# Kernel tuning notes

Measured on AMD Instinct MI355X. Metric: run time of the kernel, lower is better.

## Reference

```python
import jax, jax.numpy as jnp
import numpy as np

N = 20000      # nodes
E = 200000     # edges
IN = 128       # in_feat
OUT = 128      # out_feat
NB = 8         # num_bases
SI = IN // NB  # submat_in = 16
SO = OUT // NB # submat_out = 16
R = 230        # num_rels
T = 365        # total_times


def setup_inputs() -> dict:
    key = jax.random.key(0)
    ks = jax.random.split(key, 11)
    h = jax.random.normal(ks[0], (N, IN), jnp.float32)
    edge_norm = jax.random.uniform(ks[1], (E, 1), jnp.float32)
    node_norm = jax.random.uniform(ks[2], (N, 1), jnp.float32)
    weight = jax.random.normal(ks[3], (R, NB * SI * SO), jnp.float32) * 0.05
    h_bias = jnp.zeros((OUT,), jnp.float32)
    loop_weight = jax.random.normal(ks[4], (IN, OUT), jnp.float32) * 0.05
    time_embed = jax.random.normal(ks[5], (T, IN), jnp.float32) * 0.05
    edge_src = jax.random.randint(ks[6], (E,), 0, N)
    edge_dst = jax.random.randint(ks[7], (E,), 0, N)
    edge_type = jax.random.randint(ks[8], (E,), 0, R)
    time_idx = jax.random.randint(ks[9], (N,), 0, T)
    return dict(h=h, edge_norm=edge_norm, node_norm=node_norm, weight=weight,
                h_bias=h_bias, loop_weight=loop_weight, time_embed=time_embed,
                edge_src=edge_src, edge_dst=edge_dst, edge_type=edge_type,
                time_idx=time_idx)


def reference(h, edge_norm, node_norm, weight, h_bias, loop_weight, time_embed,
              edge_src, edge_dst, edge_type, time_idx):
    # self-loop message
    loop_message = h @ loop_weight                              # [N, OUT]
    # msg_func: per-edge relation weight gather + block-diagonal bmm
    W_e = weight[edge_type].reshape(-1, NB, SI, SO)             # [E, NB, SI, SO]
    src = h[edge_src].reshape(-1, NB, SI)                       # [E, NB, SI]
    msg = jnp.einsum('ebi,ebio->ebo', src, W_e).reshape(-1, OUT)  # [E, OUT]
    msg = msg * edge_norm
    # fn.sum aggregation over destination nodes
    agg = jax.ops.segment_sum(msg, edge_dst, num_segments=N)    # [N, OUT]
    # apply_func: scale by node norm, then bias + self loop + activation
    node_repr = agg * node_norm
    node_repr = node_repr + h_bias + loop_message
    node_repr = jax.nn.relu(node_repr)
    # get_time_embedding: per-node time embedding gather
    time_embedding = time_embed[time_idx]                       # [N, IN]
    return node_repr, time_embedding
```

## Files before the change

### kernel.cpp

```cpp
#include <hip/hip_runtime.h>
#include <hip/hip_bf16.h>

#define N 20000
#define E 200000
#define IN 128
#define OUT 128
#define NB 8
#define SI 16
#define SO 16
#define R 230
#define T 365

__device__ float g_agg[(size_t)N * OUT];
__device__ int   g_deg[N];
__device__ int   g_off[N + 1];
__device__ int   g_cur[N];
__device__ int   g_srt_src[E];
__device__ int   g_srt_typ[E];
__device__ float g_srt_nrm[E];

__global__ void zero_deg_kernel() {
    int i = blockIdx.x * blockDim.x + threadIdx.x;
    if (i < N) g_deg[i] = 0;
}

__global__ void count_kernel(const int* __restrict__ edge_dst) {
    int e = blockIdx.x * blockDim.x + threadIdx.x;
    if (e < E) atomicAdd(&g_deg[edge_dst[e]], 1);
}

__global__ __launch_bounds__(1024) void scan_kernel() {
    __shared__ int part[1024];
    const int t = threadIdx.x;
    const int base = t * 20;
    int csum = 0;
    int d[20];
#pragma unroll
    for (int k = 0; k < 20; ++k) {
        int idx = base + k;
        d[k] = (idx < N) ? g_deg[idx] : 0;
        csum += d[k];
    }
    part[t] = csum;
    __syncthreads();
    for (int off = 1; off < 1024; off <<= 1) {
        int v = (t >= off) ? part[t - off] : 0;
        __syncthreads();
        part[t] += v;
        __syncthreads();
    }
    int run = part[t] - csum;
#pragma unroll
    for (int k = 0; k < 20; ++k) {
        int idx = base + k;
        if (idx < N) {
            g_off[idx] = run;
            g_cur[idx] = run;
            run += d[k];
        }
    }
    if (t == 1023) g_off[N] = part[1023];
}

__global__ void scatter_kernel(const int* __restrict__ edge_src,
                               const int* __restrict__ edge_dst,
                               const int* __restrict__ edge_type,
                               const float* __restrict__ edge_norm) {
    int e = blockIdx.x * blockDim.x + threadIdx.x;
    if (e >= E) return;
    int pos = atomicAdd(&g_cur[edge_dst[e]], 1);
    g_srt_src[pos] = edge_src[e];
    g_srt_typ[pos] = edge_type[e];
    g_srt_nrm[pos] = edge_norm[e];
}

__global__ __launch_bounds__(128) void agg_kernel(const float* __restrict__ h,
                                                  const float* __restrict__ weight) {
    const int n    = blockIdx.x;
    const int tid  = threadIdx.x;
    const int el   = tid >> 5;
    const int slot = tid & 31;
    const int b    = slot >> 2;
    const int ol0  = (slot & 3) << 2;
    const int j0 = g_off[n], j1 = g_off[n + 1];

    float4 acc = make_float4(0.f, 0.f, 0.f, 0.f);
    for (int j = j0 + el; j < j1; j += 4) {
        int   s  = g_srt_src[j];
        int   r  = g_srt_typ[j];
        float nr = g_srt_nrm[j];
        const float4* hp = reinterpret_cast<const float4*>(h + (long)s * IN + b * SI);
        const float4* wp = reinterpret_cast<const float4*>(
            weight + (long)r * (NB * SI * SO) + b * (SI * SO) + ol0);
        float4 d = make_float4(0.f, 0.f, 0.f, 0.f);
#pragma unroll
        for (int q = 0; q < 4; ++q) {
            float4 hq = hp[q];
            float4 w0 = wp[(4 * q + 0) * 4];
            float4 w1 = wp[(4 * q + 1) * 4];
            float4 w2 = wp[(4 * q + 2) * 4];
            float4 w3 = wp[(4 * q + 3) * 4];
            d.x = fmaf(hq.x, w0.x, d.x); d.y = fmaf(hq.x, w0.y, d.y);
            d.z = fmaf(hq.x, w0.z, d.z); d.w = fmaf(hq.x, w0.w, d.w);
            d.x = fmaf(hq.y, w1.x, d.x); d.y = fmaf(hq.y, w1.y, d.y);
            d.z = fmaf(hq.y, w1.z, d.z); d.w = fmaf(hq.y, w1.w, d.w);
            d.x = fmaf(hq.z, w2.x, d.x); d.y = fmaf(hq.z, w2.y, d.y);
            d.z = fmaf(hq.z, w2.z, d.z); d.w = fmaf(hq.z, w2.w, d.w);
            d.x = fmaf(hq.w, w3.x, d.x); d.y = fmaf(hq.w, w3.y, d.y);
            d.z = fmaf(hq.w, w3.z, d.z); d.w = fmaf(hq.w, w3.w, d.w);
        }
        acc.x = fmaf(d.x, nr, acc.x);
        acc.y = fmaf(d.y, nr, acc.y);
        acc.z = fmaf(d.z, nr, acc.z);
        acc.w = fmaf(d.w, nr, acc.w);
    }

    __shared__ float4 red[128];
    red[tid] = acc;
    __syncthreads();
    if (tid < 64) {
        float4 a = red[tid], c = red[tid + 64];
        a.x += c.x; a.y += c.y; a.z += c.z; a.w += c.w;
        red[tid] = a;
    }
    __syncthreads();
    if (tid < 32) {
        float4 a = red[tid], c = red[tid + 32];
        a.x += c.x; a.y += c.y; a.z += c.z; a.w += c.w;
        reinterpret_cast<float4*>(g_agg)[(long)n * 32 + tid] = a;
    }
}

__global__ __launch_bounds__(128) void node_kernel(
        const float* __restrict__ h,
        const float* __restrict__ node_norm,
        const float* __restrict__ h_bias,
        const float* __restrict__ loop_weight,
        const float* __restrict__ time_embed,
        const int* __restrict__ time_idx,
        float* __restrict__ out) {
    __shared__ float hsm[IN * 16];
    const int tid  = threadIdx.x;
    const int base = blockIdx.x * 16;

    for (int k = tid; k < 16 * IN; k += 128) {
        int nl = k >> 7;
        int i  = k & 127;
        hsm[i * 16 + nl] = h[(long)(base + nl) * IN + i];
    }
    __syncthreads();

    float acc[16];
#pragma unroll
    for (int nl = 0; nl < 16; ++nl) acc[nl] = 0.f;

    for (int i = 0; i < IN; ++i) {
        float w = loop_weight[(long)i * OUT + tid];
        const float4* hp = reinterpret_cast<const float4*>(&hsm[i * 16]);
#pragma unroll
        for (int q = 0; q < 4; ++q) {
            float4 hv = hp[q];
            acc[q * 4 + 0] = fmaf(hv.x, w, acc[q * 4 + 0]);
            acc[q * 4 + 1] = fmaf(hv.y, w, acc[q * 4 + 1]);
            acc[q * 4 + 2] = fmaf(hv.z, w, acc[q * 4 + 2]);
            acc[q * 4 + 3] = fmaf(hv.w, w, acc[q * 4 + 3]);
        }
    }

    float bias = h_bias[tid];
#pragma unroll
    for (int nl = 0; nl < 16; ++nl) {
        int n = base + nl;
        float v = g_agg[(long)n * OUT + tid] * node_norm[n] + bias + acc[nl];
        out[(long)n * OUT + tid] = fmaxf(v, 0.f);
        out[(long)N * OUT + (long)n * IN + tid] =
            time_embed[(long)time_idx[n] * IN + tid];
    }
}

extern "C" void kernel_launch(void* const* d_in, const int* in_sizes, int n_in,
                              void* d_out, int out_size, void* d_ws, size_t ws_size,
                              hipStream_t stream) {
    const float* h           = (const float*)d_in[0];
    const float* edge_norm   = (const float*)d_in[1];
    const float* node_norm   = (const float*)d_in[2];
    const float* weight      = (const float*)d_in[3];
    const float* h_bias      = (const float*)d_in[4];
    const float* loop_weight = (const float*)d_in[5];
    const float* time_embed  = (const float*)d_in[6];
    const int*   edge_src    = (const int*)d_in[7];
    const int*   edge_dst    = (const int*)d_in[8];
    const int*   edge_type   = (const int*)d_in[9];
    const int*   time_idx    = (const int*)d_in[10];
    float* out = (float*)d_out;

    zero_deg_kernel<<<(N + 255) / 256, 256, 0, stream>>>();
    count_kernel<<<(E + 255) / 256, 256, 0, stream>>>(edge_dst);
    scan_kernel<<<1, 1024, 0, stream>>>();
    scatter_kernel<<<(E + 255) / 256, 256, 0, stream>>>(
        edge_src, edge_dst, edge_type, edge_norm);

    agg_kernel<<<N, 128, 0, stream>>>(h, weight);

    node_kernel<<<N / 16, 128, 0, stream>>>(
        h, node_norm, h_bias, loop_weight, time_embed, time_idx, out);
}
```

Baseline: 242.1 us.

## Group edges by relation to reuse weights, materialize messages, then aggregate

Adds a second counting sort of edges by relation type. A new message kernel keeps each relation's weight slice in registers and computes per-edge messages into a global E x OUT buffer at the destination-sorted position. The aggregation kernel then only sums precomputed messages. This removes the repeated per-edge weight gathers, but adds a 100MB message buffer write and read, extra atomics, and a serial per-relation scan.

```diff
diff --git a/kernel.cpp b/kernel.cpp
--- a/kernel.cpp
+++ b/kernel.cpp
@@ -10,23 +10,32 @@
 #define SO 16
 #define R 230
 #define T 365
-
+#define MSG_CHUNKS 8
+
+__device__ float g_msg[(size_t)E * OUT];
 __device__ float g_agg[(size_t)N * OUT];
 __device__ int   g_deg[N];
 __device__ int   g_off[N + 1];
 __device__ int   g_cur[N];
-__device__ int   g_srt_src[E];
-__device__ int   g_srt_typ[E];
-__device__ float g_srt_nrm[E];
-
-__global__ void zero_deg_kernel() {
+__device__ int   g_rdeg[R];
+__device__ int   g_roff[R + 1];
+__device__ int   g_rcur[R];
+__device__ int   g_rsrc[E];
+__device__ int   g_rpos[E];
+__device__ float g_rnrm[E];
+
+__global__ void zero_kernel() {
     int i = blockIdx.x * blockDim.x + threadIdx.x;
     if (i < N) g_deg[i] = 0;
-}
-
-__global__ void count_kernel(const int* __restrict__ edge_dst) {
+    if (i < R) g_rdeg[i] = 0;
+}
+
+__global__ void count_kernel(const int* __restrict__ edge_dst,
+                             const int* __restrict__ edge_type) {
     int e = blockIdx.x * blockDim.x + threadIdx.x;
-    if (e < E) atomicAdd(&g_deg[edge_dst[e]], 1);
+    if (e >= E) return;
+    atomicAdd(&g_deg[edge_dst[e]], 1);
+    atomicAdd(&g_rdeg[edge_type[e]], 1);
 }
 
 __global__ __launch_bounds__(1024) void scan_kernel() {
@@ -60,6 +69,15 @@
         }
     }
     if (t == 1023) g_off[N] = part[1023];
+    if (t == 0) {
+        int acc = 0;
+        for (int r = 0; r < R; ++r) {
+            g_roff[r] = acc;
+            g_rcur[r] = acc;
+            acc += g_rdeg[r];
+        }
+        g_roff[R] = acc;
+    }
 }
 
 __global__ void scatter_kernel(const int* __restrict__ edge_src,
@@ -68,53 +86,73 @@
                                const float* __restrict__ edge_norm) {
     int e = blockIdx.x * blockDim.x + threadIdx.x;
     if (e >= E) return;
-    int pos = atomicAdd(&g_cur[edge_dst[e]], 1);
-    g_srt_src[pos] = edge_src[e];
-    g_srt_typ[pos] = edge_type[e];
-    g_srt_nrm[pos] = edge_norm[e];
-}
-
-__global__ __launch_bounds__(128) void agg_kernel(const float* __restrict__ h,
+    int pd = atomicAdd(&g_cur[edge_dst[e]], 1);
+    int pr = atomicAdd(&g_rcur[edge_type[e]], 1);
+    g_rsrc[pr] = edge_src[e];
+    g_rpos[pr] = pd;
+    g_rnrm[pr] = edge_norm[e];
+}
+
+__global__ __launch_bounds__(256) void msg_kernel(const float* __restrict__ h,
                                                   const float* __restrict__ weight) {
-    const int n    = blockIdx.x;
-    const int tid  = threadIdx.x;
-    const int el   = tid >> 5;
-    const int slot = tid & 31;
-    const int b    = slot >> 2;
-    const int ol0  = (slot & 3) << 2;
+    const int r = blockIdx.x / MSG_CHUNKS;
+    const int c = blockIdx.x % MSG_CHUNKS;
+    const int t = threadIdx.x;
+    const int g = t >> 7;
+    const int o = t & 127;
+    const int b = o >> 4, ol = o & 15;
+
+    const int j0 = g_roff[r], j1 = g_roff[r + 1];
+    const int len = j1 - j0;
+    const int s0 = j0 + (int)(((long)len * c) / MSG_CHUNKS);
+    const int s1 = j0 + (int)(((long)len * (c + 1)) / MSG_CHUNKS);
+
+    float w[SI];
+#pragma unroll
+    for (int i = 0; i < SI; ++i)
+        w[i] = weight[(long)r * (NB * SI * SO) + b * (SI * SO) + i * SO + ol];
+
+    __shared__ float hs[2][IN];
+    for (int base = s0; base < s1; base += 2) {
+        int j = base + g;
+        bool valid = (j < s1);
+        int s = 0, pd = 0;
+        float nr = 0.f;
+        if (valid) {
+            s  = g_rsrc[j];
+            pd = g_rpos[j];
+            nr = g_rnrm[j];
+            hs[g][o] = h[(long)s * IN + o];
+        }
+        __syncthreads();
+        if (valid) {
+            const float4* hp = reinterpret_cast<const float4*>(&hs[g][b * SI]);
+            float dot = 0.f;
+#pragma unroll
+            for (int q = 0; q < 4; ++q) {
+                float4 hv = hp[q];
+                dot = fmaf(hv.x, w[4 * q + 0], dot);
+                dot = fmaf(hv.y, w[4 * q + 1], dot);
+                dot = fmaf(hv.z, w[4 * q + 2], dot);
+                dot = fmaf(hv.w, w[4 * q + 3], dot);
+            }
+            g_msg[(long)pd * OUT + o] = dot * nr;
+        }
+        __syncthreads();
+    }
+}
+
+__global__ __launch_bounds__(128) void agg_kernel() {
+    const int n   = blockIdx.x;
+    const int tid = threadIdx.x;
+    const int el  = tid >> 5;
+    const int q   = tid & 31;
     const int j0 = g_off[n], j1 = g_off[n + 1];
-
     float4 acc = make_float4(0.f, 0.f, 0.f, 0.f);
     for (int j = j0 + el; j < j1; j += 4) {
-        int   s  = g_srt_src[j];
-        int   r  = g_srt_typ[j];
-        float nr = g_srt_nrm[j];
-        const float4* hp = reinterpret_cast<const float4*>(h + (long)s * IN + b * SI);
-        const float4* wp = reinterpret_cast<const float4*>(
-            weight + (long)r * (NB * SI * SO) + b * (SI * SO) + ol0);
-        float4 d = make_float4(0.f, 0.f, 0.f, 0.f);
-#pragma unroll
-        for (int q = 0; q < 4; ++q) {
-            float4 hq = hp[q];
-            float4 w0 = wp[(4 * q + 0) * 4];
-            float4 w1 = wp[(4 * q + 1) * 4];
-            float4 w2 = wp[(4 * q + 2) * 4];
-            float4 w3 = wp[(4 * q + 3) * 4];
-            d.x = fmaf(hq.x, w0.x, d.x); d.y = fmaf(hq.x, w0.y, d.y);
-            d.z = fmaf(hq.x, w0.z, d.z); d.w = fmaf(hq.x, w0.w, d.w);
-            d.x = fmaf(hq.y, w1.x, d.x); d.y = fmaf(hq.y, w1.y, d.y);
-            d.z = fmaf(hq.y, w1.z, d.z); d.w = fmaf(hq.y, w1.w, d.w);
-            d.x = fmaf(hq.z, w2.x, d.x); d.y = fmaf(hq.z, w2.y, d.y);
-            d.z = fmaf(hq.z, w2.z, d.z); d.w = fmaf(hq.z, w2.w, d.w);
-            d.x = fmaf(hq.w, w3.x, d.x); d.y = fmaf(hq.w, w3.y, d.y);
-            d.z = fmaf(hq.w, w3.z, d.z); d.w = fmaf(hq.w, w3.w, d.w);
-        }
-        acc.x = fmaf(d.x, nr, acc.x);
-        acc.y = fmaf(d.y, nr, acc.y);
-        acc.z = fmaf(d.z, nr, acc.z);
-        acc.w = fmaf(d.w, nr, acc.w);
-    }
-
+        float4 v = reinterpret_cast<const float4*>(g_msg)[(long)j * 32 + q];
+        acc.x += v.x; acc.y += v.y; acc.z += v.z; acc.w += v.w;
+    }
     __shared__ float4 red[128];
     red[tid] = acc;
     __syncthreads();
@@ -194,13 +232,14 @@
     const int*   time_idx    = (const int*)d_in[10];
     float* out = (float*)d_out;
 
-    zero_deg_kernel<<<(N + 255) / 256, 256, 0, stream>>>();
-    count_kernel<<<(E + 255) / 256, 256, 0, stream>>>(edge_dst);
+    zero_kernel<<<(N + 255) / 256, 256, 0, stream>>>();
+    count_kernel<<<(E + 255) / 256, 256, 0, stream>>>(edge_dst, edge_type);
     scan_kernel<<<1, 1024, 0, stream>>>();
     scatter_kernel<<<(E + 255) / 256, 256, 0, stream>>>(
         edge_src, edge_dst, edge_type, edge_norm);
 
-    agg_kernel<<<N, 128, 0, stream>>>(h, weight);
+    msg_kernel<<<R * MSG_CHUNKS, 256, 0, stream>>>(h, weight);
+    agg_kernel<<<N, 128, 0, stream>>>();
 
     node_kernel<<<N / 16, 128, 0, stream>>>(
         h, node_norm, h_bias, loop_weight, time_embed, time_idx, out);
```

Result: slower. 443.6 us (+83.3%).
